# Kernel optimization log

Hardware: AMD Instinct MI355X
Metric: run time of the kernel (lower is better)

The kernel has to match this reference:

```python
import jax, jax.numpy as jnp
import numpy as np

T, N, E, F, H = 8, 50000, 800000, 128, 128
NHEADS = 4
DH = H // NHEADS


def setup_inputs() -> dict:
    key = jax.random.key(0)
    ks = jax.random.split(key, 24)

    def rn(k, shape, scale=0.05):
        return jax.random.normal(k, shape, dtype=jnp.float32) * scale

    return {
        "xs": rn(ks[0], (T, N, F), 1.0),
        "edge_index": jax.random.randint(ks[1], (T, 2, E), 0, N, dtype=jnp.int32),
        # SAGEConv layers: out = mean_aggr(x_src) @ Wl + x @ Wr + b (bias on lin_l only)
        "Wl1": rn(ks[2], (F, H)), "Wr1": rn(ks[3], (F, H)), "b1": jnp.zeros((H,), jnp.float32),
        "Wl2": rn(ks[4], (H, H)), "Wr2": rn(ks[5], (H, H)), "b2": jnp.zeros((H,), jnp.float32),
        "Wl3": rn(ks[6], (H, H)), "Wr3": rn(ks[7], (H, H)), "b3": jnp.zeros((H,), jnp.float32),
        # MultiheadAttention (applied as x @ W, i.e. W = torch_weight.T)
        "Wq": rn(ks[8], (H, H)), "bq": jnp.zeros((H,), jnp.float32),
        "Wk": rn(ks[9], (H, H)), "bk": jnp.zeros((H,), jnp.float32),
        "Wv": rn(ks[10], (H, H)), "bv": jnp.zeros((H,), jnp.float32),
        "Wo": rn(ks[11], (H, H)), "bo": jnp.zeros((H,), jnp.float32),
        # MLP head
        "Wh1": rn(ks[12], (H, H // 2)), "bh1": jnp.zeros((H // 2,), jnp.float32),
        "Wh2": rn(ks[13], (H // 2, 1)), "bh2": jnp.zeros((1,), jnp.float32),
    }


def _sage(x, src, dst, Wl, Wr, b):
    # gather messages from source nodes, mean-aggregate at destinations
    msg = x[src]                                               # [E, F]
    ssum = jax.ops.segment_sum(msg, dst, num_segments=N)       # [N, F]
    cnt = jax.ops.segment_sum(jnp.ones((msg.shape[0],), x.dtype), dst, num_segments=N)
    agg = ssum / jnp.maximum(cnt, 1.0)[:, None]
    return agg @ Wl + x @ Wr + b


def reference(xs, edge_index, Wl1, Wr1, b1, Wl2, Wr2, b2, Wl3, Wr3, b3,
              Wq, bq, Wk, bk, Wv, bv, Wo, bo, Wh1, bh1, Wh2, bh2):
    def step(_, xe):
        x, ei = xe
        src, dst = ei[0], ei[1]
        h = jax.nn.relu(_sage(x, src, dst, Wl1, Wr1, b1))  # dropout = identity (eval)
        h = jax.nn.relu(_sage(h, src, dst, Wl2, Wr2, b2))
        h = jax.nn.relu(_sage(h, src, dst, Wl3, Wr3, b3))
        return None, h.mean(axis=0)                        # mean pool over nodes -> [H]

    _, pooled = jax.lax.scan(step, None, (xs, edge_index))  # [T, H]

    seq = pooled[None]                                      # [1, T, H]
    q = (seq @ Wq + bq).reshape(1, T, NHEADS, DH).transpose(0, 2, 1, 3)
    k = (seq @ Wk + bk).reshape(1, T, NHEADS, DH).transpose(0, 2, 1, 3)
    v = (seq @ Wv + bv).reshape(1, T, NHEADS, DH).transpose(0, 2, 1, 3)
    scale = jnp.float32(1.0 / np.sqrt(DH))
    attn = jax.nn.softmax(jnp.einsum('bhqd,bhkd->bhqk', q, k) * scale, axis=-1)
    o = jnp.einsum('bhqk,bhkd->bhqd', attn, v).transpose(0, 2, 1, 3).reshape(1, T, H)
    o = o @ Wo + bo                                         # [1, T, H]

    z = o[:, -1, :]                                         # [1, H] (last timestep)
    h1 = jax.nn.relu(z @ Wh1 + bh1)
    logits = jax.nn.sigmoid(h1 @ Wh2 + bh2)                 # [1, 1]
    return logits.squeeze(-1)                               # [1]
```

## Files before the change

### kernel.cpp

```cpp
#include <hip/hip_runtime.h>
#include <math.h>

#define TT 8
#define NN 50000
#define EE 800000
#define FF 128
#define HH 128

#define NB 98
#define BSHIFT 9
#define CAP 14336
#define RS 16384

typedef __attribute__((ext_vector_type(8))) short short8;
typedef __attribute__((ext_vector_type(4))) float f32x4;
typedef __attribute__((ext_vector_type(2))) float f32x2;
typedef unsigned char uchar;

__device__ inline unsigned bf16pack(float x) {
    unsigned u = __float_as_uint(x);
    return (u + 0x7fffu + ((u >> 16) & 1u)) >> 16;
}
__device__ inline unsigned pack2bf16_trunc(float lo, float hi) {
    return (__float_as_uint(hi) & 0xffff0000u) | (__float_as_uint(lo) >> 16);
}


__global__ __launch_bounds__(256) void cast_x_kernel(const float4* __restrict__ in,
                                                     int* __restrict__ out, long n4) {
    long i = (long)blockIdx.x * 256 + threadIdx.x;
    if (i < n4) {
        float4 v = in[i];
        int w = __builtin_amdgcn_cvt_pk_fp8_f32(v.x, v.y, 0, false);
        w = __builtin_amdgcn_cvt_pk_fp8_f32(v.z, v.w, w, true);
        out[i] = w;
    }
}

__global__ __launch_bounds__(256) void wprep_kernel(const float* __restrict__ Wl,
                                                    const float* __restrict__ Wr,
                                                    ushort* __restrict__ Bt) {
    int n = blockIdx.x;
    int k = threadIdx.x;
    float v = (k < 128) ? Wl[k * HH + n] : Wr[(k - 128) * HH + n];
    Bt[n * 256 + k] = (ushort)bf16pack(v);
}


__global__ __launch_bounds__(256) void partA_kernel(const int* __restrict__ ei,
                                                    int* __restrict__ bucketCursor,
                                                    uint2* __restrict__ pairs) {
    __shared__ int hist[NB];
    __shared__ int base[NB];
    int t = blockIdx.y, tid = threadIdx.x;
    const int* src = ei + (size_t)t * 2 * EE;
    const int* dst = src + EE;
    int e0 = blockIdx.x * 2048;
    int s[8], d[8];
#pragma unroll
    for (int k = 0; k < 8; k++) {
        int e = e0 + k * 256 + tid;
        bool ok = e < EE;
        s[k] = ok ? src[e] : -1;
        d[k] = ok ? dst[e] : -1;
    }
    if (tid < NB) hist[tid] = 0;
    __syncthreads();
#pragma unroll
    for (int k = 0; k < 8; k++)
        if (d[k] >= 0) atomicAdd(&hist[d[k] >> BSHIFT], 1);
    __syncthreads();
    if (tid < NB) {
        base[tid] = atomicAdd(&bucketCursor[t * NB + tid], hist[tid]);
        hist[tid] = 0;
    }
    __syncthreads();
#pragma unroll
    for (int k = 0; k < 8; k++)
        if (d[k] >= 0) {
            int b = d[k] >> BSHIFT;
            int idx = base[b] + atomicAdd(&hist[b], 1);
            if (idx < CAP)
                pairs[((size_t)t * NB + b) * RS + idx] = make_uint2((unsigned)s[k], (unsigned)d[k]);
        }
}

__global__ void bscan_kernel(const int* __restrict__ bucketCursor,
                             int* __restrict__ bucketBase) {
    int t = threadIdx.x;
    if (t < TT) {
        int run = 0;
        for (int b = 0; b < NB; b++) {
            bucketBase[t * NB + b] = run;
            int c = bucketCursor[t * NB + b];
            run += (c > CAP ? CAP : c);
        }
    }
}

__global__ __launch_bounds__(256) void partB_kernel(const uint2* __restrict__ pairs,
                                                    const int* __restrict__ bucketCursor,
                                                    const int* __restrict__ bucketBase,
                                                    int* __restrict__ cnt,
                                                    int* __restrict__ rowstart,
                                                    int* __restrict__ srcs_sorted) {
    __shared__ int hist[512];
    __shared__ int offs[512];
    __shared__ int sh2[256];
    __shared__ int staged[CAP];
    int t = blockIdx.y, b = blockIdx.x, tid = threadIdx.x;
    int n0 = b << BSHIFT;
    int nn = NN - n0; if (nn > 512) nn = 512;
    int cb = bucketCursor[t * NB + b]; if (cb > CAP) cb = CAP;
    int ebase = bucketBase[t * NB + b];
    const uint2* P = pairs + ((size_t)t * NB + b) * RS;

    hist[tid] = 0; hist[tid + 256] = 0;
    __syncthreads();
    for (int i = tid; i < cb; i += 256) atomicAdd(&hist[(int)P[i].y - n0], 1);
    __syncthreads();
    int a0 = hist[2 * tid], a1 = hist[2 * tid + 1];
    sh2[tid] = a0 + a1;
    __syncthreads();
    for (int off = 1; off < 256; off <<= 1) {
        int v = (tid >= off) ? sh2[tid - off] : 0;
        __syncthreads();
        sh2[tid] += v;
        __syncthreads();
    }
    int excl = sh2[tid] - (a0 + a1);
    offs[2 * tid] = excl;
    offs[2 * tid + 1] = excl + a0;
    __syncthreads();
    for (int i = tid; i < nn; i += 256) {
        cnt[(size_t)t * NN + n0 + i] = hist[i];
        rowstart[(size_t)t * NN + n0 + i] = ebase + offs[i];
    }
    __syncthreads();
    hist[tid] = offs[tid]; hist[tid + 256] = offs[tid + 256];
    __syncthreads();
    for (int i = tid; i < cb; i += 256) {
        uint2 p = P[i];
        int slot = atomicAdd(&hist[(int)p.y - n0], 1);
        staged[slot] = (int)p.x;
    }
    __syncthreads();
    int* outp = srcs_sorted + (size_t)t * EE + ebase;
    for (int i = tid; i < cb; i += 256) outp[i] = staged[i];
}

__global__ __launch_bounds__(256) void agg_kernel(const uchar* __restrict__ xin,
                                                  const int* __restrict__ srcs_sorted,
                                                  const int* __restrict__ rowstart,
                                                  const int* __restrict__ cnt,
                                                  uchar* __restrict__ aggq) {
    int node = blockIdx.x * 4 + (threadIdx.x >> 6);
    if (node >= NN) return;
    int lane = threadIdx.x & 63;
    int quad = lane >> 4, l15 = lane & 15;
    int rs = rowstart[node];
    int c = cnt[node];
    const uint2* x2 = (const uint2*)xin;
    float a0 = 0.f, a1 = 0.f, a2 = 0.f, a3 = 0.f, a4 = 0.f, a5 = 0.f, a6 = 0.f, a7 = 0.f;
    int j = quad;
    for (; j + 4 < c; j += 8) {
        int s0 = srcs_sorted[rs + j];
        int s1 = srcs_sorted[rs + j + 4];
        uint2 v0 = x2[(size_t)s0 * 16 + l15];
        uint2 v1 = x2[(size_t)s1 * 16 + l15];
        f32x2 p;
        p = __builtin_amdgcn_cvt_pk_f32_fp8((int)v0.x, false); a0 += p.x; a1 += p.y;
        p = __builtin_amdgcn_cvt_pk_f32_fp8((int)v0.x, true);  a2 += p.x; a3 += p.y;
        p = __builtin_amdgcn_cvt_pk_f32_fp8((int)v0.y, false); a4 += p.x; a5 += p.y;
        p = __builtin_amdgcn_cvt_pk_f32_fp8((int)v0.y, true);  a6 += p.x; a7 += p.y;
        p = __builtin_amdgcn_cvt_pk_f32_fp8((int)v1.x, false); a0 += p.x; a1 += p.y;
        p = __builtin_amdgcn_cvt_pk_f32_fp8((int)v1.x, true);  a2 += p.x; a3 += p.y;
        p = __builtin_amdgcn_cvt_pk_f32_fp8((int)v1.y, false); a4 += p.x; a5 += p.y;
        p = __builtin_amdgcn_cvt_pk_f32_fp8((int)v1.y, true);  a6 += p.x; a7 += p.y;
    }
    if (j < c) {
        uint2 v0 = x2[(size_t)srcs_sorted[rs + j] * 16 + l15];
        f32x2 p;
        p = __builtin_amdgcn_cvt_pk_f32_fp8((int)v0.x, false); a0 += p.x; a1 += p.y;
        p = __builtin_amdgcn_cvt_pk_f32_fp8((int)v0.x, true);  a2 += p.x; a3 += p.y;
        p = __builtin_amdgcn_cvt_pk_f32_fp8((int)v0.y, false); a4 += p.x; a5 += p.y;
        p = __builtin_amdgcn_cvt_pk_f32_fp8((int)v0.y, true);  a6 += p.x; a7 += p.y;
    }
#pragma unroll
    for (int o = 16; o <= 32; o <<= 1) {
        a0 += __shfl_xor(a0, o, 64);
        a1 += __shfl_xor(a1, o, 64);
        a2 += __shfl_xor(a2, o, 64);
        a3 += __shfl_xor(a3, o, 64);
        a4 += __shfl_xor(a4, o, 64);
        a5 += __shfl_xor(a5, o, 64);
        a6 += __shfl_xor(a6, o, 64);
        a7 += __shfl_xor(a7, o, 64);
    }
    if (quad == 0) {
        float inv = 1.0f / (float)(c > 0 ? c : 1);
        int w0 = __builtin_amdgcn_cvt_pk_fp8_f32(a0 * inv, a1 * inv, 0, false);
        w0 = __builtin_amdgcn_cvt_pk_fp8_f32(a2 * inv, a3 * inv, w0, true);
        int w1 = __builtin_amdgcn_cvt_pk_fp8_f32(a4 * inv, a5 * inv, 0, false);
        w1 = __builtin_amdgcn_cvt_pk_fp8_f32(a6 * inv, a7 * inv, w1, true);
        ((uint2*)aggq)[(size_t)node * 16 + l15] = make_uint2((unsigned)w0, (unsigned)w1);
    }
}

__global__ __launch_bounds__(256) void gemm_mfma_kernel(const uchar* __restrict__ AaggF,
                                                        const uchar* __restrict__ AxF,
                                                        const ushort* __restrict__ Bt,
                                                        const float* __restrict__ bias,
                                                        uchar* __restrict__ outF) {
    extern __shared__ char smem[];
    ushort* As = (ushort*)smem;
    ushort* Bs = (ushort*)(smem + 128 * 72 * 2);
    uchar* Cs = (uchar*)smem;

    size_t toff = (size_t)blockIdx.y * NN * HH;
    const uchar* Aagg = AaggF + toff;
    const uchar* Ax = AxF + toff;
    uchar* out = outF + toff;

    int tid = threadIdx.x;
    int row0 = blockIdx.x * 128;
    int lane = tid & 63, wave = tid >> 6;
    int wm = wave >> 1, wn = wave & 1;
    int l15 = lane & 15, quad = lane >> 4;

    f32x4 acc[4][4];
#pragma unroll
    for (int i = 0; i < 4; i++)
#pragma unroll
        for (int j = 0; j < 4; j++) acc[i][j] = (f32x4){0.f, 0.f, 0.f, 0.f};

    int srow = tid >> 1;
    int cb = (tid & 1) * 32;
    int grow = row0 + srow;

    for (int s = 0; s < 4; s++) {
        const uchar* Asrc = (s < 2) ? Aagg : Ax;
        int acol = (s & 1) * 64 + cb;
        uint4 r0 = make_uint4(0u, 0u, 0u, 0u), r1 = r0;
        if (grow < NN) {
            const uchar* ap = Asrc + (size_t)grow * HH + acol;
            r0 = *(const uint4*)ap;
            r1 = *(const uint4*)(ap + 16);
        }
        const ushort* bp = Bt + srow * 256 + s * 64 + cb;
        uint4 bv[4];
#pragma unroll
        for (int c = 0; c < 4; c++) bv[c] = *(const uint4*)(bp + c * 8);

        unsigned w[8] = {r0.x, r0.y, r0.z, r0.w, r1.x, r1.y, r1.z, r1.w};
        unsigned u[16];
#pragma unroll
        for (int wi = 0; wi < 8; wi++) {
            f32x2 lo = __builtin_amdgcn_cvt_pk_f32_fp8((int)w[wi], false);
            f32x2 hi = __builtin_amdgcn_cvt_pk_f32_fp8((int)w[wi], true);
            u[2 * wi] = pack2bf16_trunc(lo.x, lo.y);
            u[2 * wi + 1] = pack2bf16_trunc(hi.x, hi.y);
        }
        __syncthreads();
#pragma unroll
        for (int c = 0; c < 4; c++)
            *(uint4*)&As[srow * 72 + cb + c * 8] =
                make_uint4(u[4 * c], u[4 * c + 1], u[4 * c + 2], u[4 * c + 3]);
#pragma unroll
        for (int c = 0; c < 4; c++) *(uint4*)&Bs[srow * 72 + cb + c * 8] = bv[c];
        __syncthreads();
#pragma unroll
        for (int ks = 0; ks < 2; ks++) {
            int k0 = ks * 32 + quad * 8;
            short8 a[4], b[4];
#pragma unroll
            for (int i = 0; i < 4; i++)
                a[i] = *(const short8*)&As[(wm * 64 + i * 16 + l15) * 72 + k0];
#pragma unroll
            for (int j = 0; j < 4; j++)
                b[j] = *(const short8*)&Bs[(wn * 64 + j * 16 + l15) * 72 + k0];
#pragma unroll
            for (int i = 0; i < 4; i++)
#pragma unroll
                for (int j = 0; j < 4; j++)
                    acc[i][j] = __builtin_amdgcn_mfma_f32_16x16x32_bf16(a[i], b[j], acc[i][j], 0, 0, 0);
        }
    }
    __syncthreads();

#pragma unroll
    for (int i = 0; i < 4; i++)
#pragma unroll
        for (int j = 0; j < 4; j++) {
            int col = wn * 64 + j * 16 + l15;
            float bb = bias[col];
#pragma unroll
            for (int r = 0; r < 4; r++) {
                int rl = wm * 64 + i * 16 + quad * 4 + r;
                float v = fmaxf(acc[i][j][r] + bb, 0.f);
                int pk = __builtin_amdgcn_cvt_pk_fp8_f32(v, 0.f, 0, false);
                Cs[rl * 144 + col] = (uchar)(pk & 0xff);
            }
        }
    __syncthreads();

    int orow = tid >> 1;
    int ocb = (tid & 1) * 64;
    if (row0 + orow < NN) {
#pragma unroll
        for (int c = 0; c < 4; c++)
            *(uint4*)&out[(size_t)(row0 + orow) * HH + ocb + c * 16] =
                *(const uint4*)&Cs[orow * 144 + ocb + c * 16];
    }
}

__global__ __launch_bounds__(256) void pool_kernel(const uchar* __restrict__ hF,
                                                   float* __restrict__ pooled) {
    int t = blockIdx.y;
    const unsigned* h = (const unsigned*)(hF + (size_t)t * NN * HH);
    int tid = threadIdx.x;
    int wave = tid >> 6, lane = tid & 63;
    int fw = lane & 31;
    int rh = lane >> 5;
    float s0 = 0.f, s1 = 0.f, s2 = 0.f, s3 = 0.f;
    for (int r = blockIdx.x * 8 + wave * 2 + rh; r < NN; r += gridDim.x * 8) {
        unsigned u = h[(size_t)r * 32 + fw];
        f32x2 lo = __builtin_amdgcn_cvt_pk_f32_fp8((int)u, false);
        f32x2 hi = __builtin_amdgcn_cvt_pk_f32_fp8((int)u, true);
        s0 += lo.x; s1 += lo.y; s2 += hi.x; s3 += hi.y;
    }
    s0 += __shfl_xor(s0, 32, 64);
    s1 += __shfl_xor(s1, 32, 64);
    s2 += __shfl_xor(s2, 32, 64);
    s3 += __shfl_xor(s3, 32, 64);
    if (lane < 32) {
        const float inv = 1.0f / (float)NN;
        atomicAdd(&pooled[t * HH + fw * 4 + 0], s0 * inv);
        atomicAdd(&pooled[t * HH + fw * 4 + 1], s1 * inv);
        atomicAdd(&pooled[t * HH + fw * 4 + 2], s2 * inv);
        atomicAdd(&pooled[t * HH + fw * 4 + 3], s3 * inv);
    }
}

__global__ __launch_bounds__(256) void head_kernel(const float* __restrict__ pooled,
                                                   const float* __restrict__ Wq, const float* __restrict__ bq,
                                                   const float* __restrict__ Wk, const float* __restrict__ bk,
                                                   const float* __restrict__ Wv, const float* __restrict__ bv,
                                                   const float* __restrict__ Wo, const float* __restrict__ bo,
                                                   const float* __restrict__ Wh1, const float* __restrict__ bh1,
                                                   const float* __restrict__ Wh2, const float* __restrict__ bh2,
                                                   float* __restrict__ out) {
    __shared__ float seq[TT * HH];
    __shared__ float kb[TT * HH];
    __shared__ float vbuf[TT * HH];
    __shared__ float q7[HH];
    __shared__ float sc[4][8];
    __shared__ float zb[HH];
    __shared__ float ob[HH];
    __shared__ float h1b[64];
    int tid = threadIdx.x;
    for (int i = tid; i < TT * HH; i += 256) seq[i] = pooled[i];
    __syncthreads();
    for (int i = tid; i < TT * HH; i += 256) {
        int t = i >> 7, h = i & 127;
        float sk = bk[h], sv = bv[h];
        for (int j = 0; j < HH; j++) {
            float s = seq[t * HH + j];
            sk += s * Wk[j * HH + h];
            sv += s * Wv[j * HH + h];
        }
        kb[i] = sk;
        vbuf[i] = sv;
    }
    if (tid < HH) {
        float sq = bq[tid];
        for (int j = 0; j < HH; j++) sq += seq[7 * HH + j] * Wq[j * HH + tid];
        q7[tid] = sq;
    }
    __syncthreads();
    if (tid < 32) {
        int g = tid >> 3, tt = tid & 7;
        float s = 0.f;
        for (int d = 0; d < 32; d++) s += q7[g * 32 + d] * kb[tt * HH + g * 32 + d];
        sc[g][tt] = s * 0.1767766952966369f;
    }
    __syncthreads();
    if (tid < 4) {
        float m = -1e30f;
        for (int i = 0; i < 8; i++) m = fmaxf(m, sc[tid][i]);
        float e[8], sum = 0.f;
        for (int i = 0; i < 8; i++) { e[i] = expf(sc[tid][i] - m); sum += e[i]; }
        for (int i = 0; i < 8; i++) sc[tid][i] = e[i] / sum;
    }
    __syncthreads();
    if (tid < HH) {
        int g = tid >> 5;
        float s = 0.f;
        for (int t = 0; t < 8; t++) s += sc[g][t] * vbuf[t * HH + tid];
        zb[tid] = s;
    }
    __syncthreads();
    if (tid < HH) {
        float s = bo[tid];
        for (int j = 0; j < HH; j++) s += zb[j] * Wo[j * HH + tid];
        ob[tid] = s;
    }
    __syncthreads();
    if (tid < 64) {
        float s = bh1[tid];
        for (int j = 0; j < HH; j++) s += ob[j] * Wh1[j * 64 + tid];
        h1b[tid] = fmaxf(s, 0.f);
    }
    __syncthreads();
    if (tid == 0) {
        float s = bh2[0];
        for (int j = 0; j < 64; j++) s += h1b[j] * Wh2[j];
        out[0] = 1.0f / (1.0f + expf(-s));
    }
}


extern "C" void kernel_launch(void* const* d_in, const int* in_sizes, int n_in,
                              void* d_out, int out_size, void* d_ws, size_t ws_size,
                              hipStream_t stream) {
    const float* xs = (const float*)d_in[0];
    const int* ei = (const int*)d_in[1];
    const float* Wl1 = (const float*)d_in[2];
    const float* Wr1 = (const float*)d_in[3];
    const float* b1 = (const float*)d_in[4];
    const float* Wl2 = (const float*)d_in[5];
    const float* Wr2 = (const float*)d_in[6];
    const float* b2 = (const float*)d_in[7];
    const float* Wl3 = (const float*)d_in[8];
    const float* Wr3 = (const float*)d_in[9];
    const float* b3 = (const float*)d_in[10];
    const float* Wq = (const float*)d_in[11];
    const float* bq = (const float*)d_in[12];
    const float* Wk = (const float*)d_in[13];
    const float* bk = (const float*)d_in[14];
    const float* Wv = (const float*)d_in[15];
    const float* bv = (const float*)d_in[16];
    const float* Wo = (const float*)d_in[17];
    const float* bo = (const float*)d_in[18];
    const float* Wh1 = (const float*)d_in[19];
    const float* bh1 = (const float*)d_in[20];
    const float* Wh2 = (const float*)d_in[21];
    const float* bh2 = (const float*)d_in[22];

    size_t off = 0;
    char* base = (char*)d_ws;
    auto carve = [&](size_t bytes) -> char* {
        char* p = base + off;
        off += (bytes + 255) & ~(size_t)255;
        return p;
    };
    int* cnt = (int*)carve((size_t)TT * NN * 4);
    int* rowstart = (int*)carve((size_t)TT * NN * 4);
    int* srcs_sorted = (int*)carve((size_t)TT * EE * 4);
    int* bucketCursor = (int*)carve((size_t)TT * NB * 4);
    int* bucketBase = (int*)carve((size_t)TT * NB * 4);
    uint2* pairs = (uint2*)carve((size_t)TT * NB * RS * 8);
    uchar* xq = (uchar*)carve((size_t)TT * NN * HH);
    uchar* aggq = (uchar*)carve((size_t)TT * NN * HH);
    uchar* h1q = (uchar*)carve((size_t)TT * NN * HH);
    uchar* h2q = (uchar*)carve((size_t)TT * NN * HH);
    ushort* Bt1 = (ushort*)carve((size_t)128 * 256 * 2);
    ushort* Bt2 = (ushort*)carve((size_t)128 * 256 * 2);
    ushort* Bt3 = (ushort*)carve((size_t)128 * 256 * 2);
    float* pooled = (float*)carve((size_t)TT * HH * 4);

    hipMemsetAsync(pooled, 0, (size_t)TT * HH * 4, stream);
    hipMemsetAsync(bucketCursor, 0, (size_t)TT * NB * 4, stream);

    long n4 = (long)TT * NN * FF / 4;
    cast_x_kernel<<<(int)((n4 + 255) / 256), 256, 0, stream>>>((const float4*)xs, (int*)xq, n4);
    wprep_kernel<<<128, 256, 0, stream>>>(Wl1, Wr1, Bt1);
    wprep_kernel<<<128, 256, 0, stream>>>(Wl2, Wr2, Bt2);
    wprep_kernel<<<128, 256, 0, stream>>>(Wl3, Wr3, Bt3);

    partA_kernel<<<dim3((EE + 2047) / 2048, TT), 256, 0, stream>>>(ei, bucketCursor, pairs);
    bscan_kernel<<<1, 64, 0, stream>>>(bucketCursor, bucketBase);
    partB_kernel<<<dim3(NB, TT), 256, 0, stream>>>(pairs, bucketCursor, bucketBase,
                                                   cnt, rowstart, srcs_sorted);

    const int gemmGrid = (NN + 127) / 128;
    const int aggGrid = (NN + 3) / 4;
    const int gemmLds = 128 * 72 * 2 * 2;

    for (int t = 0; t < TT; t++)
        agg_kernel<<<aggGrid, 256, 0, stream>>>(xq + (size_t)t * NN * HH,
                                                srcs_sorted + (size_t)t * EE,
                                                rowstart + (size_t)t * NN,
                                                cnt + (size_t)t * NN,
                                                aggq + (size_t)t * NN * HH);
    gemm_mfma_kernel<<<dim3(gemmGrid, TT), 256, gemmLds, stream>>>(aggq, xq, Bt1, b1, h1q);
    for (int t = 0; t < TT; t++)
        agg_kernel<<<aggGrid, 256, 0, stream>>>(h1q + (size_t)t * NN * HH,
                                                srcs_sorted + (size_t)t * EE,
                                                rowstart + (size_t)t * NN,
                                                cnt + (size_t)t * NN,
                                                aggq + (size_t)t * NN * HH);
    gemm_mfma_kernel<<<dim3(gemmGrid, TT), 256, gemmLds, stream>>>(aggq, h1q, Bt2, b2, h2q);
    for (int t = 0; t < TT; t++)
        agg_kernel<<<aggGrid, 256, 0, stream>>>(h2q + (size_t)t * NN * HH,
                                                srcs_sorted + (size_t)t * EE,
                                                rowstart + (size_t)t * NN,
                                                cnt + (size_t)t * NN,
                                                aggq + (size_t)t * NN * HH);
    gemm_mfma_kernel<<<dim3(gemmGrid, TT), 256, gemmLds, stream>>>(aggq, h2q, Bt3, b3, h1q);

    pool_kernel<<<dim3(64, TT), 256, 0, stream>>>(h1q, pooled);

    head_kernel<<<1, 256, 0, stream>>>(pooled, Wq, bq, Wk, bk, Wv, bv, Wo, bo,
                                       Wh1, bh1, Wh2, bh2, (float*)d_out);
}
```

Measured before the change: 1.389 ms.

## Batch per-timestep launches, fuse mean-pool into last GEMM, prefetch A tiles

The per-timestep agg launches become one 2D-grid launch, and the three weight-prep launches become one. The last-layer GEMM gets a POOL template variant that reduces ReLU outputs into column sums in shared memory and atomically adds them to pooled. This removes the separate pool kernel and the write and re-read of the final hidden activations. The GEMM also prefetches the next A-tile into registers while computing the current stage, which adds register pressure and changes the float summation order of the pooled mean.

```diff
diff --git a/kernel.cpp b/kernel.cpp
--- a/kernel.cpp
+++ b/kernel.cpp
@@ -37,9 +37,15 @@
     }
 }
 
-__global__ __launch_bounds__(256) void wprep_kernel(const float* __restrict__ Wl,
-                                                    const float* __restrict__ Wr,
-                                                    ushort* __restrict__ Bt) {
+__global__ __launch_bounds__(256) void wprep_kernel(const float* __restrict__ Wl1, const float* __restrict__ Wr1,
+                                                    const float* __restrict__ Wl2, const float* __restrict__ Wr2,
+                                                    const float* __restrict__ Wl3, const float* __restrict__ Wr3,
+                                                    ushort* __restrict__ Bt1, ushort* __restrict__ Bt2,
+                                                    ushort* __restrict__ Bt3) {
+    int which = blockIdx.y;
+    const float* Wl = (which == 0) ? Wl1 : (which == 1) ? Wl2 : Wl3;
+    const float* Wr = (which == 0) ? Wr1 : (which == 1) ? Wr2 : Wr3;
+    ushort* Bt = (which == 0) ? Bt1 : (which == 1) ? Bt2 : Bt3;
     int n = blockIdx.x;
     int k = threadIdx.x;
     float v = (k < 128) ? Wl[k * HH + n] : Wr[(k - 128) * HH + n];
@@ -149,18 +155,20 @@
     for (int i = tid; i < cb; i += 256) outp[i] = staged[i];
 }
 
-__global__ __launch_bounds__(256) void agg_kernel(const uchar* __restrict__ xin,
-                                                  const int* __restrict__ srcs_sorted,
-                                                  const int* __restrict__ rowstart,
-                                                  const int* __restrict__ cnt,
-                                                  uchar* __restrict__ aggq) {
+__global__ __launch_bounds__(256) void agg_kernel(const uchar* __restrict__ xinF,
+                                                  const int* __restrict__ srcs_sortedF,
+                                                  const int* __restrict__ rowstartF,
+                                                  const int* __restrict__ cntF,
+                                                  uchar* __restrict__ aggqF) {
+    int t = blockIdx.y;
     int node = blockIdx.x * 4 + (threadIdx.x >> 6);
     if (node >= NN) return;
     int lane = threadIdx.x & 63;
     int quad = lane >> 4, l15 = lane & 15;
-    int rs = rowstart[node];
-    int c = cnt[node];
-    const uint2* x2 = (const uint2*)xin;
+    const int* srcs_sorted = srcs_sortedF + (size_t)t * EE;
+    int rs = rowstartF[(size_t)t * NN + node];
+    int c = cntF[(size_t)t * NN + node];
+    const uint2* x2 = (const uint2*)(xinF + (size_t)t * NN * HH);
     float a0 = 0.f, a1 = 0.f, a2 = 0.f, a3 = 0.f, a4 = 0.f, a5 = 0.f, a6 = 0.f, a7 = 0.f;
     int j = quad;
     for (; j + 4 < c; j += 8) {
@@ -203,15 +211,18 @@
         w0 = __builtin_amdgcn_cvt_pk_fp8_f32(a2 * inv, a3 * inv, w0, true);
         int w1 = __builtin_amdgcn_cvt_pk_fp8_f32(a4 * inv, a5 * inv, 0, false);
         w1 = __builtin_amdgcn_cvt_pk_fp8_f32(a6 * inv, a7 * inv, w1, true);
-        ((uint2*)aggq)[(size_t)node * 16 + l15] = make_uint2((unsigned)w0, (unsigned)w1);
-    }
-}
-
+        ((uint2*)(aggqF + (size_t)t * NN * HH))[(size_t)node * 16 + l15] =
+            make_uint2((unsigned)w0, (unsigned)w1);
+    }
+}
+
+template <int POOL>
 __global__ __launch_bounds__(256) void gemm_mfma_kernel(const uchar* __restrict__ AaggF,
                                                         const uchar* __restrict__ AxF,
                                                         const ushort* __restrict__ Bt,
                                                         const float* __restrict__ bias,
-                                                        uchar* __restrict__ outF) {
+                                                        uchar* __restrict__ outF,
+                                                        float* __restrict__ pooled) {
     extern __shared__ char smem[];
     ushort* As = (ushort*)smem;
     ushort* Bs = (ushort*)(smem + 128 * 72 * 2);
@@ -238,20 +249,14 @@
     int cb = (tid & 1) * 32;
     int grow = row0 + srow;
 
+    uint4 r0 = make_uint4(0u, 0u, 0u, 0u), r1 = r0;
+    if (grow < NN) {
+        const uchar* ap = Aagg + (size_t)grow * HH + cb;
+        r0 = *(const uint4*)ap;
+        r1 = *(const uint4*)(ap + 16);
+    }
+
     for (int s = 0; s < 4; s++) {
-        const uchar* Asrc = (s < 2) ? Aagg : Ax;
-        int acol = (s & 1) * 64 + cb;
-        uint4 r0 = make_uint4(0u, 0u, 0u, 0u), r1 = r0;
-        if (grow < NN) {
-            const uchar* ap = Asrc + (size_t)grow * HH + acol;
-            r0 = *(const uint4*)ap;
-            r1 = *(const uint4*)(ap + 16);
-        }
-        const ushort* bp = Bt + srow * 256 + s * 64 + cb;
-        uint4 bv[4];
-#pragma unroll
-        for (int c = 0; c < 4; c++) bv[c] = *(const uint4*)(bp + c * 8);
-
         unsigned w[8] = {r0.x, r0.y, r0.z, r0.w, r1.x, r1.y, r1.z, r1.w};
         unsigned u[16];
 #pragma unroll
@@ -261,6 +266,10 @@
             u[2 * wi] = pack2bf16_trunc(lo.x, lo.y);
             u[2 * wi + 1] = pack2bf16_trunc(hi.x, hi.y);
         }
+        const ushort* bp = Bt + srow * 256 + s * 64 + cb;
+        uint4 bv[4];
+#pragma unroll
+        for (int c = 0; c < 4; c++) bv[c] = *(const uint4*)(bp + c * 8);
         __syncthreads();
 #pragma unroll
         for (int c = 0; c < 4; c++)
@@ -269,6 +278,17 @@
 #pragma unroll
         for (int c = 0; c < 4; c++) *(uint4*)&Bs[srow * 72 + cb + c * 8] = bv[c];
         __syncthreads();
+        if (s < 3) {
+            const uchar* Asrc = (s + 1 < 2) ? Aagg : Ax;
+            int acol = ((s + 1) & 1) * 64 + cb;
+            r0 = make_uint4(0u, 0u, 0u, 0u);
+            r1 = r0;
+            if (grow < NN) {
+                const uchar* ap = Asrc + (size_t)grow * HH + acol;
+                r0 = *(const uint4*)ap;
+                r1 = *(const uint4*)(ap + 16);
+            }
+        }
 #pragma unroll
         for (int ks = 0; ks < 2; ks++) {
             int k0 = ks * 32 + quad * 8;
@@ -288,57 +308,55 @@
     }
     __syncthreads();
 
-#pragma unroll
-    for (int i = 0; i < 4; i++)
+    if (POOL == 0) {
+#pragma unroll
+        for (int i = 0; i < 4; i++)
+#pragma unroll
+            for (int j = 0; j < 4; j++) {
+                int col = wn * 64 + j * 16 + l15;
+                float bb = bias[col];
+#pragma unroll
+                for (int r = 0; r < 4; r++) {
+                    int rl = wm * 64 + i * 16 + quad * 4 + r;
+                    float v = fmaxf(acc[i][j][r] + bb, 0.f);
+                    int pk = __builtin_amdgcn_cvt_pk_fp8_f32(v, 0.f, 0, false);
+                    Cs[rl * 144 + col] = (uchar)(pk & 0xff);
+                }
+            }
+        __syncthreads();
+
+        int orow = tid >> 1;
+        int ocb = (tid & 1) * 64;
+        if (row0 + orow < NN) {
+#pragma unroll
+            for (int c = 0; c < 4; c++)
+                *(uint4*)&out[(size_t)(row0 + orow) * HH + ocb + c * 16] =
+                    *(const uint4*)&Cs[orow * 144 + ocb + c * 16];
+        }
+    } else {
+        float* colsum = (float*)smem;
+        if (tid < HH) colsum[tid] = 0.f;
+        __syncthreads();
 #pragma unroll
         for (int j = 0; j < 4; j++) {
             int col = wn * 64 + j * 16 + l15;
             float bb = bias[col];
-#pragma unroll
-            for (int r = 0; r < 4; r++) {
-                int rl = wm * 64 + i * 16 + quad * 4 + r;
-                float v = fmaxf(acc[i][j][r] + bb, 0.f);
-                int pk = __builtin_amdgcn_cvt_pk_fp8_f32(v, 0.f, 0, false);
-                Cs[rl * 144 + col] = (uchar)(pk & 0xff);
-            }
-        }
-    __syncthreads();
-
-    int orow = tid >> 1;
-    int ocb = (tid & 1) * 64;
-    if (row0 + orow < NN) {
-#pragma unroll
-        for (int c = 0; c < 4; c++)
-            *(uint4*)&out[(size_t)(row0 + orow) * HH + ocb + c * 16] =
-                *(const uint4*)&Cs[orow * 144 + ocb + c * 16];
-    }
-}
-
-__global__ __launch_bounds__(256) void pool_kernel(const uchar* __restrict__ hF,
-                                                   float* __restrict__ pooled) {
-    int t = blockIdx.y;
-    const unsigned* h = (const unsigned*)(hF + (size_t)t * NN * HH);
-    int tid = threadIdx.x;
-    int wave = tid >> 6, lane = tid & 63;
-    int fw = lane & 31;
-    int rh = lane >> 5;
-    float s0 = 0.f, s1 = 0.f, s2 = 0.f, s3 = 0.f;
-    for (int r = blockIdx.x * 8 + wave * 2 + rh; r < NN; r += gridDim.x * 8) {
-        unsigned u = h[(size_t)r * 32 + fw];
-        f32x2 lo = __builtin_amdgcn_cvt_pk_f32_fp8((int)u, false);
-        f32x2 hi = __builtin_amdgcn_cvt_pk_f32_fp8((int)u, true);
-        s0 += lo.x; s1 += lo.y; s2 += hi.x; s3 += hi.y;
-    }
-    s0 += __shfl_xor(s0, 32, 64);
-    s1 += __shfl_xor(s1, 32, 64);
-    s2 += __shfl_xor(s2, 32, 64);
-    s3 += __shfl_xor(s3, 32, 64);
-    if (lane < 32) {
-        const float inv = 1.0f / (float)NN;
-        atomicAdd(&pooled[t * HH + fw * 4 + 0], s0 * inv);
-        atomicAdd(&pooled[t * HH + fw * 4 + 1], s1 * inv);
-        atomicAdd(&pooled[t * HH + fw * 4 + 2], s2 * inv);
-        atomicAdd(&pooled[t * HH + fw * 4 + 3], s3 * inv);
+            float ps = 0.f;
+#pragma unroll
+            for (int i = 0; i < 4; i++)
+#pragma unroll
+                for (int r = 0; r < 4; r++) {
+                    int rl = wm * 64 + i * 16 + quad * 4 + r;
+                    float v = fmaxf(acc[i][j][r] + bb, 0.f);
+                    ps += (row0 + rl < NN) ? v : 0.f;
+                }
+            ps += __shfl_xor(ps, 16, 64);
+            ps += __shfl_xor(ps, 32, 64);
+            if (quad == 0) atomicAdd(&colsum[col], ps);
+        }
+        __syncthreads();
+        if (tid < HH)
+            atomicAdd(&pooled[blockIdx.y * HH + tid], colsum[tid] * (1.0f / (float)NN));
     }
 }
 
@@ -474,9 +492,7 @@
 
     long n4 = (long)TT * NN * FF / 4;
     cast_x_kernel<<<(int)((n4 + 255) / 256), 256, 0, stream>>>((const float4*)xs, (int*)xq, n4);
-    wprep_kernel<<<128, 256, 0, stream>>>(Wl1, Wr1, Bt1);
-    wprep_kernel<<<128, 256, 0, stream>>>(Wl2, Wr2, Bt2);
-    wprep_kernel<<<128, 256, 0, stream>>>(Wl3, Wr3, Bt3);
+    wprep_kernel<<<dim3(128, 3), 256, 0, stream>>>(Wl1, Wr1, Wl2, Wr2, Wl3, Wr3, Bt1, Bt2, Bt3);
 
     partA_kernel<<<dim3((EE + 2047) / 2048, TT), 256, 0, stream>>>(ei, bucketCursor, pairs);
     bscan_kernel<<<1, 64, 0, stream>>>(bucketCursor, bucketBase);
@@ -487,29 +503,12 @@
     const int aggGrid = (NN + 3) / 4;
     const int gemmLds = 128 * 72 * 2 * 2;
 
-    for (int t = 0; t < TT; t++)
-        agg_kernel<<<aggGrid, 256, 0, stream>>>(xq + (size_t)t * NN * HH,
-                                                srcs_sorted + (size_t)t * EE,
-                                                rowstart + (size_t)t * NN,
-                                                cnt + (size_t)t * NN,
-                                                aggq + (size_t)t * NN * HH);
-    gemm_mfma_kernel<<<dim3(gemmGrid, TT), 256, gemmLds, stream>>>(aggq, xq, Bt1, b1, h1q);
-    for (int t = 0; t < TT; t++)
-        agg_kernel<<<aggGrid, 256, 0, stream>>>(h1q + (size_t)t * NN * HH,
-                                                srcs_sorted + (size_t)t * EE,
-                                                rowstart + (size_t)t * NN,
-                                                cnt + (size_t)t * NN,
-                                                aggq + (size_t)t * NN * HH);
-    gemm_mfma_kernel<<<dim3(gemmGrid, TT), 256, gemmLds, stream>>>(aggq, h1q, Bt2, b2, h2q);
-    for (int t = 0; t < TT; t++)
-        agg_kernel<<<aggGrid, 256, 0, stream>>>(h2q + (size_t)t * NN * HH,
-                                                srcs_sorted + (size_t)t * EE,
-                                                rowstart + (size_t)t * NN,
-                                                cnt + (size_t)t * NN,
-                                                aggq + (size_t)t * NN * HH);
-    gemm_mfma_kernel<<<dim3(gemmGrid, TT), 256, gemmLds, stream>>>(aggq, h2q, Bt3, b3, h1q);
-
-    pool_kernel<<<dim3(64, TT), 256, 0, stream>>>(h1q, pooled);
+    agg_kernel<<<dim3(aggGrid, TT), 256, 0, stream>>>(xq, srcs_sorted, rowstart, cnt, aggq);
+    gemm_mfma_kernel<0><<<dim3(gemmGrid, TT), 256, gemmLds, stream>>>(aggq, xq, Bt1, b1, h1q, nullptr);
+    agg_kernel<<<dim3(aggGrid, TT), 256, 0, stream>>>(h1q, srcs_sorted, rowstart, cnt, aggq);
+    gemm_mfma_kernel<0><<<dim3(gemmGrid, TT), 256, gemmLds, stream>>>(aggq, h1q, Bt2, b2, h2q, nullptr);
+    agg_kernel<<<dim3(aggGrid, TT), 256, 0, stream>>>(h2q, srcs_sorted, rowstart, cnt, aggq);
+    gemm_mfma_kernel<1><<<dim3(gemmGrid, TT), 256, gemmLds, stream>>>(aggq, h2q, Bt3, b3, h1q, pooled);
 
     head_kernel<<<1, 256, 0, stream>>>(pooled, Wq, bq, Wk, bk, Wv, bv, Wo, bo,
                                        Wh1, bh1, Wh2, bh2, (float*)d_out);
```

New measurement: 1.246 ms. 1.11x faster.
